# Optimization experiments

Hardware: AMD Instinct MI355X
Metric: run time of the kernel (lower is better)

## Reference

```python
import jax, jax.numpy as jnp
import numpy as np

B, C, N = 4, 256, 4096
OUT = 256
TEMP = OUT ** 0.5  # temperature = sqrt(out_channel)


def setup_inputs() -> dict:
    key = jax.random.key(0)
    kx, kxx, kq, kk, kv = jax.random.split(key, 5)
    x = jax.random.normal(kx, (B, C, N), dtype=jnp.float32)
    xx = jax.random.normal(kxx, (B, C, N), dtype=jnp.float32)
    # Conv1d(in, out, kernel=1, bias=False) weights, squeezed to (out, in)
    s = 1.0 / np.sqrt(C)
    Wq = jax.random.uniform(kq, (OUT, C), jnp.float32, -s, s)
    Wk = jax.random.uniform(kk, (OUT, C), jnp.float32, -s, s)
    Wv = jax.random.uniform(kv, (OUT, C), jnp.float32, -s, s)
    return {"x": x, "xx": xx, "Wq": Wq, "Wk": Wk, "Wv": Wv}


def reference(x, xx, Wq, Wk, Wv):
    # 1x1 conv == per-point linear: (out,in) x (b,in,n) -> (b,out,n)
    q = jnp.einsum('oc,bcn->bon', Wq, x)
    k = jnp.einsum('oc,bcn->bon', Wk, xx)
    v = jnp.einsum('oc,bcn->bon', Wv, xx)
    # attn = (q^T / temp) @ k : (B, N, N)
    attn = jax.nn.softmax(jnp.einsum('bon,bom->bnm', q, k) / TEMP, axis=-1)
    # dropout is identity in eval mode
    # y = attn @ v^T -> (B, N, OUT); returned transposed to (B, OUT, N)
    y = jnp.einsum('bnm,bom->bon', attn, v)
    return y
```

## Files before the change

kernel.cpp:

```cpp
#include <hip/hip_runtime.h>
#include <hip/hip_bf16.h>


typedef __attribute__((ext_vector_type(8))) short bf16x8;
typedef __attribute__((ext_vector_type(4))) float f32x4;
typedef __attribute__((ext_vector_type(4))) short short4t;

constexpr int B_ = 4;
constexpr int C_ = 256;
constexpr int N_ = 4096;
constexpr int O_ = 256;
constexpr float INV_TEMP = 1.0f / 16.0f;
constexpr int NIT = 64;

__device__ __forceinline__ short f2bf(float f) {
  union { float f; unsigned u; } v; v.f = f;
  unsigned r = v.u + 0x7fffu + ((v.u >> 16) & 1u);
  return (short)(r >> 16);
}

__device__ __forceinline__ void dma16(const short* g, short* l) {
  __builtin_amdgcn_global_load_lds(
      (const __attribute__((address_space(1))) unsigned int*)g,
      (__attribute__((address_space(3))) unsigned int*)l, 16, 0, 0);
}

__global__ void wcvt(const float* __restrict__ Wq, const float* __restrict__ Wk,
                     const float* __restrict__ Wv, short* __restrict__ wb) {
  int i = blockIdx.x * 256 + threadIdx.x;
  int mat = i >> 16, off = i & 65535;
  const float* W = (mat == 0) ? Wq : (mat == 1 ? Wk : Wv);
  wb[i] = f2bf(W[off]);
}

__global__ __launch_bounds__(256, 2) void qkv_proj(
    const float* __restrict__ x, const float* __restrict__ xx,
    const short* __restrict__ wb,
    short* __restrict__ qg, short* __restrict__ kt, short* __restrict__ vt) {
  const int n0  = blockIdx.x * 64;
  const int b   = blockIdx.y;
  const int mat = blockIdx.z;
  const float* src = (mat == 0) ? x : xx;
  const short* W   = wb + mat * 65536;
  const int tid = threadIdx.x;
  const int w = tid >> 6, lane = tid & 63;
  const int g = lane >> 4, c16 = lane & 15;

  __shared__ __align__(16) short xs[64][264];

  {
    const int n = tid & 63, cq = tid >> 6;
    const float* sp = src + (size_t)b * C_ * N_ + n0 + n;
#pragma unroll
    for (int rep = 0; rep < 16; ++rep) {
      int c = rep * 16 + cq * 4;
      short4t s4;
#pragma unroll
      for (int j = 0; j < 4; ++j) s4[j] = f2bf(sp[(size_t)(c + j) * N_]);
      *(short4t*)&xs[n][c] = s4;
    }
  }
  __syncthreads();

  f32x4 acc[4][4];
#pragma unroll
  for (int i = 0; i < 4; ++i)
#pragma unroll
    for (int j = 0; j < 4; ++j) acc[i][j] = (f32x4){0.f, 0.f, 0.f, 0.f};

#pragma unroll
  for (int ko = 0; ko < 8; ++ko) {
    bf16x8 wfr[4], xfr[4];
#pragma unroll
    for (int ot = 0; ot < 4; ++ot)
      wfr[ot] = *(const bf16x8*)&W[(w * 64 + ot * 16 + c16) * C_ + ko * 32 + g * 8];
#pragma unroll
    for (int nt = 0; nt < 4; ++nt)
      xfr[nt] = *(const bf16x8*)&xs[nt * 16 + c16][ko * 32 + g * 8];
    if (mat < 2) {
#pragma unroll
      for (int ot = 0; ot < 4; ++ot)
#pragma unroll
        for (int nt = 0; nt < 4; ++nt)
          acc[ot][nt] = __builtin_amdgcn_mfma_f32_16x16x32_bf16(
              wfr[ot], xfr[nt], acc[ot][nt], 0, 0, 0);
    } else {
#pragma unroll
      for (int mt = 0; mt < 4; ++mt)
#pragma unroll
        for (int ot = 0; ot < 4; ++ot)
          acc[mt][ot] = __builtin_amdgcn_mfma_f32_16x16x32_bf16(
              xfr[mt], wfr[ot], acc[mt][ot], 0, 0, 0);
    }
  }

  __syncthreads();
  short* ob = &xs[0][0];

  if (mat == 0) {
#pragma unroll
    for (int ot = 0; ot < 4; ++ot)
#pragma unroll
      for (int nt = 0; nt < 4; ++nt) {
        int f = (nt * 16 + c16) * 256 + w * 64 + ot * 16 + g * 4;
        short4t s;
        s[0] = f2bf(acc[ot][nt][0] * INV_TEMP);
        s[1] = f2bf(acc[ot][nt][1] * INV_TEMP);
        s[2] = f2bf(acc[ot][nt][2] * INV_TEMP);
        s[3] = f2bf(acc[ot][nt][3] * INV_TEMP);
        *(short4t*)&ob[f] = s;
      }
  } else if (mat == 1) {
#pragma unroll
    for (int ot = 0; ot < 4; ++ot)
#pragma unroll
      for (int nt = 0; nt < 4; ++nt) {
        int koo = w * 2 + (ot >> 1);
        int pos = (((ot & 1) * 2 + (g >> 1)) ^ ((c16 >> 1) & 3));
        int f = nt * 4096 + koo * 512 + c16 * 32 + pos * 8 + (g & 1) * 4;
        short4t s;
        s[0] = f2bf(acc[ot][nt][0]);
        s[1] = f2bf(acc[ot][nt][1]);
        s[2] = f2bf(acc[ot][nt][2]);
        s[3] = f2bf(acc[ot][nt][3]);
        *(short4t*)&ob[f] = s;
      }
  } else {
#pragma unroll
    for (int mt = 0; mt < 4; ++mt)
#pragma unroll
      for (int ot = 0; ot < 4; ++ot) {
        int o = w * 64 + ot * 16 + c16;
        int pos = (mt * 2 + (g >> 1)) ^ (o & 7);
        int f = o * 64 + pos * 8 + (g & 1) * 4;
        short4t s;
        s[0] = f2bf(acc[mt][ot][0]);
        s[1] = f2bf(acc[mt][ot][1]);
        s[2] = f2bf(acc[mt][ot][2]);
        s[3] = f2bf(acc[mt][ot][3]);
        *(short4t*)&ob[f] = s;
      }
  }
  __syncthreads();

  short* dst = (mat == 0) ? qg + ((size_t)b * N_ + n0) * O_
             : (mat == 1) ? kt + (size_t)(b * 256 + (n0 >> 4)) * 4096
                          : vt + (size_t)(b * 64 + (n0 >> 6)) * 16384;
  const uint4* s4 = (const uint4*)ob;
  uint4* d4 = (uint4*)dst;
#pragma unroll
  for (int j = 0; j < 8; ++j) d4[j * 256 + tid] = s4[j * 256 + tid];
}

__global__ __launch_bounds__(512, 2) void flash_attn(
    const short* __restrict__ qg, const short* __restrict__ kt,
    const short* __restrict__ vt, float* __restrict__ out) {
  const int xg = blockIdx.x;
  const int b  = xg >> 1;
  const int n0 = (((xg & 1) << 5) + blockIdx.y) * 64;
  const int tid = threadIdx.x;
  const int w = tid >> 6, lane = tid & 63;
  const int g = lane >> 4, c16 = lane & 15;
  const bool prod = (w < 4);
  const int pw = w & 3;

  __shared__ short kb[2][16384];
  __shared__ short vb[2][16384];
  __shared__ short ps[2][64][72];
  __shared__ float lsum[4][64];

  const short* ktb = kt + (size_t)b * N_ * O_;
  const short* vtb = vt + (size_t)b * N_ * O_;

  bf16x8 qf[4][8];
  float lrun[4] = {0.f, 0.f, 0.f, 0.f};
  f32x4 oacc[4][4];
#pragma unroll
  for (int i = 0; i < 4; ++i)
#pragma unroll
    for (int j = 0; j < 4; ++j) oacc[i][j] = (f32x4){0.f, 0.f, 0.f, 0.f};

  if (prod) {
#pragma unroll
    for (int nt = 0; nt < 4; ++nt) {
      const short* qrow =
          qg + (size_t)(b * N_ + n0 + nt * 16 + c16) * O_ + g * 8;
#pragma unroll
      for (int ko = 0; ko < 8; ++ko)
        qf[nt][ko] = *(const bf16x8*)(qrow + ko * 32);
    }
    const short* src = ktb + (size_t)pw * 4096;
#pragma unroll
    for (int j = 0; j < 8; ++j)
      dma16(src + j * 512 + lane * 8, &kb[0][pw * 4096 + j * 512]);
  }
  __syncthreads();

  const int sw = (g ^ ((c16 >> 1) & 3)) * 8;

  for (int i = 0; i <= NIT; ++i) {
    if (prod) {
      if (i < NIT) {
        if (i + 1 < NIT) {
          const short* src = ktb + (size_t)(4 * (i + 1) + pw) * 4096;
          short* dst = &kb[(i + 1) & 1][pw * 4096];
#pragma unroll
          for (int j = 0; j < 8; ++j)
            dma16(src + j * 512 + lane * 8, dst + j * 512);
        }
        const short* ksl = &kb[i & 1][pw * 4096];
        f32x4 sacc[4];
#pragma unroll
        for (int nt = 0; nt < 4; ++nt) sacc[nt] = (f32x4){0.f, 0.f, 0.f, 0.f};
#pragma unroll
        for (int ko = 0; ko < 8; ++ko) {
          bf16x8 kf = *(const bf16x8*)&ksl[(ko * 16 + c16) * 32 + sw];
#pragma unroll
          for (int nt = 0; nt < 4; ++nt)
            sacc[nt] = __builtin_amdgcn_mfma_f32_16x16x32_bf16(
                kf, qf[nt][ko], sacc[nt], 0, 0, 0);
        }
#pragma unroll
        for (int nt = 0; nt < 4; ++nt) {
          short4t pb;
          float rs = 0.f;
#pragma unroll
          for (int r = 0; r < 4; ++r) {
            float p = __expf(sacc[nt][r]);
            rs += p;
            pb[r] = f2bf(p);
          }
          lrun[nt] += rs;
          *(short4t*)&ps[i & 1][nt * 16 + c16][pw * 16 + g * 4] = pb;
        }
      }
    } else {
      if (i < NIT) {
        const short* src = vtb + (size_t)i * 16384 + pw * 4096;
        short* dst = &vb[i & 1][pw * 4096];
#pragma unroll
        for (int j = 0; j < 8; ++j)
          dma16(src + j * 512 + lane * 8, dst + j * 512);
      }
      if (i > 0) {
        const int pb_ = (i - 1) & 1;
#pragma unroll
        for (int kk = 0; kk < 2; ++kk) {
          bf16x8 pf[4];
#pragma unroll
          for (int nt = 0; nt < 4; ++nt)
            pf[nt] = *(const bf16x8*)&ps[pb_][nt * 16 + c16][kk * 32 + g * 8];
#pragma unroll
          for (int ot = 0; ot < 4; ++ot) {
            int pos = (kk * 4 + g) ^ (c16 & 7);
            bf16x8 vf = *(const bf16x8*)
                &vb[pb_][(pw * 64 + ot * 16 + c16) * 64 + pos * 8];
#pragma unroll
            for (int nt = 0; nt < 4; ++nt)
              oacc[ot][nt] = __builtin_amdgcn_mfma_f32_16x16x32_bf16(
                  vf, pf[nt], oacc[ot][nt], 0, 0, 0);
          }
        }
      }
    }
    __syncthreads();
  }

  if (prod) {
#pragma unroll
    for (int nt = 0; nt < 4; ++nt) {
      float v = lrun[nt];
      v += __shfl_xor(v, 16);
      v += __shfl_xor(v, 32);
      if (lane < 16) lsum[pw][nt * 16 + lane] = v;
    }
  }
  __syncthreads();
  if (!prod) {
#pragma unroll
    for (int nt = 0; nt < 4; ++nt) {
      const int nl = nt * 16 + c16;
      float l = lsum[0][nl] + lsum[1][nl] + lsum[2][nl] + lsum[3][nl];
      float li = 1.0f / l;
#pragma unroll
      for (int ot = 0; ot < 4; ++ot) {
        float* op = out + ((size_t)b * O_ + pw * 64 + ot * 16 + g * 4) * N_ +
                    n0 + nl;
#pragma unroll
        for (int r = 0; r < 4; ++r)
          op[(size_t)r * N_] = oacc[ot][nt][r] * li;
      }
    }
  }
}

extern "C" void kernel_launch(void* const* d_in, const int* in_sizes, int n_in,
                              void* d_out, int out_size, void* d_ws,
                              size_t ws_size, hipStream_t stream) {
  const float* x  = (const float*)d_in[0];
  const float* xx = (const float*)d_in[1];
  const float* Wq = (const float*)d_in[2];
  const float* Wk = (const float*)d_in[3];
  const float* Wv = (const float*)d_in[4];
  float* out = (float*)d_out;

  short* qg = (short*)d_ws;
  short* kt = qg + (size_t)B_ * N_ * O_;
  short* vt = kt + (size_t)B_ * N_ * O_;
  short* wb = vt + (size_t)B_ * N_ * O_;

  wcvt<<<768, 256, 0, stream>>>(Wq, Wk, Wv, wb);
  qkv_proj<<<dim3(N_ / 64, B_, 3), 256, 0, stream>>>(x, xx, wb, qg, kt, vt);
  flash_attn<<<dim3(8, 32), 512, 0, stream>>>(qg, kt, vt, out);
}
```

Before: 207.3 us.

## Fuse weight conversion, QKV projection and flash attention into one cooperative kernel

Result: slower. 254.7 us (+22.9%).

```diff
diff --git a/kernel.cpp b/kernel.cpp
--- a/kernel.cpp
+++ b/kernel.cpp
@@ -1,6 +1,9 @@
 #include <hip/hip_runtime.h>
 #include <hip/hip_bf16.h>
-
+#include <hip/hip_cooperative_groups.h>
+
+
+namespace cg = cooperative_groups;
 
 typedef __attribute__((ext_vector_type(8))) short bf16x8;
 typedef __attribute__((ext_vector_type(4))) float f32x4;
@@ -19,155 +22,178 @@
   return (short)(r >> 16);
 }
 
-__device__ __forceinline__ void dma16(const short* g, short* l) {
+__device__ __forceinline__ void dma16(const void* g, void* l) {
   __builtin_amdgcn_global_load_lds(
       (const __attribute__((address_space(1))) unsigned int*)g,
       (__attribute__((address_space(3))) unsigned int*)l, 16, 0, 0);
 }
 
-__global__ void wcvt(const float* __restrict__ Wq, const float* __restrict__ Wk,
-                     const float* __restrict__ Wv, short* __restrict__ wb) {
-  int i = blockIdx.x * 256 + threadIdx.x;
-  int mat = i >> 16, off = i & 65535;
-  const float* W = (mat == 0) ? Wq : (mat == 1 ? Wk : Wv);
-  wb[i] = f2bf(W[off]);
-}
-
-__global__ __launch_bounds__(256, 2) void qkv_proj(
-    const float* __restrict__ x, const float* __restrict__ xx,
-    const short* __restrict__ wb,
-    short* __restrict__ qg, short* __restrict__ kt, short* __restrict__ vt) {
-  const int n0  = blockIdx.x * 64;
-  const int b   = blockIdx.y;
-  const int mat = blockIdx.z;
-  const float* src = (mat == 0) ? x : xx;
-  const short* W   = wb + mat * 65536;
-  const int tid = threadIdx.x;
-  const int w = tid >> 6, lane = tid & 63;
-  const int g = lane >> 4, c16 = lane & 15;
-
-  __shared__ __align__(16) short xs[64][264];
-
-  {
-    const int n = tid & 63, cq = tid >> 6;
-    const float* sp = src + (size_t)b * C_ * N_ + n0 + n;
-#pragma unroll
-    for (int rep = 0; rep < 16; ++rep) {
-      int c = rep * 16 + cq * 4;
-      short4t s4;
-#pragma unroll
-      for (int j = 0; j < 4; ++j) s4[j] = f2bf(sp[(size_t)(c + j) * N_]);
-      *(short4t*)&xs[n][c] = s4;
-    }
-  }
-  __syncthreads();
-
-  f32x4 acc[4][4];
-#pragma unroll
-  for (int i = 0; i < 4; ++i)
-#pragma unroll
-    for (int j = 0; j < 4; ++j) acc[i][j] = (f32x4){0.f, 0.f, 0.f, 0.f};
-
+__device__ __forceinline__ void proj_gemm(
+    const float* __restrict__ Wm, float ws, int swap, const short (*xs)[264],
+    int W4, int oh, int g, int c16, f32x4* a) {
+#pragma unroll
+  for (int i = 0; i < 8; ++i) a[i] = (f32x4){0.f, 0.f, 0.f, 0.f};
 #pragma unroll
   for (int ko = 0; ko < 8; ++ko) {
-    bf16x8 wfr[4], xfr[4];
-#pragma unroll
-    for (int ot = 0; ot < 4; ++ot)
-      wfr[ot] = *(const bf16x8*)&W[(w * 64 + ot * 16 + c16) * C_ + ko * 32 + g * 8];
+    bf16x8 wfr[2], xfr[4];
+#pragma unroll
+    for (int otl = 0; otl < 2; ++otl) {
+      const float* wp = Wm +
+          (size_t)(W4 * 64 + (oh * 2 + otl) * 16 + c16) * C_ + ko * 32 + g * 8;
+      float4 f0 = *(const float4*)wp;
+      float4 f1 = *(const float4*)(wp + 4);
+      bf16x8 t;
+      t[0] = f2bf(f0.x * ws); t[1] = f2bf(f0.y * ws);
+      t[2] = f2bf(f0.z * ws); t[3] = f2bf(f0.w * ws);
+      t[4] = f2bf(f1.x * ws); t[5] = f2bf(f1.y * ws);
+      t[6] = f2bf(f1.z * ws); t[7] = f2bf(f1.w * ws);
+      wfr[otl] = t;
+    }
 #pragma unroll
     for (int nt = 0; nt < 4; ++nt)
       xfr[nt] = *(const bf16x8*)&xs[nt * 16 + c16][ko * 32 + g * 8];
-    if (mat < 2) {
-#pragma unroll
-      for (int ot = 0; ot < 4; ++ot)
+    if (!swap) {
+#pragma unroll
+      for (int otl = 0; otl < 2; ++otl)
 #pragma unroll
         for (int nt = 0; nt < 4; ++nt)
-          acc[ot][nt] = __builtin_amdgcn_mfma_f32_16x16x32_bf16(
-              wfr[ot], xfr[nt], acc[ot][nt], 0, 0, 0);
+          a[otl * 4 + nt] = __builtin_amdgcn_mfma_f32_16x16x32_bf16(
+              wfr[otl], xfr[nt], a[otl * 4 + nt], 0, 0, 0);
     } else {
 #pragma unroll
       for (int mt = 0; mt < 4; ++mt)
 #pragma unroll
-        for (int ot = 0; ot < 4; ++ot)
-          acc[mt][ot] = __builtin_amdgcn_mfma_f32_16x16x32_bf16(
-              xfr[mt], wfr[ot], acc[mt][ot], 0, 0, 0);
-    }
-  }
-
-  __syncthreads();
-  short* ob = &xs[0][0];
-
-  if (mat == 0) {
-#pragma unroll
-    for (int ot = 0; ot < 4; ++ot)
-#pragma unroll
-      for (int nt = 0; nt < 4; ++nt) {
-        int f = (nt * 16 + c16) * 256 + w * 64 + ot * 16 + g * 4;
-        short4t s;
-        s[0] = f2bf(acc[ot][nt][0] * INV_TEMP);
-        s[1] = f2bf(acc[ot][nt][1] * INV_TEMP);
-        s[2] = f2bf(acc[ot][nt][2] * INV_TEMP);
-        s[3] = f2bf(acc[ot][nt][3] * INV_TEMP);
-        *(short4t*)&ob[f] = s;
-      }
-  } else if (mat == 1) {
-#pragma unroll
-    for (int ot = 0; ot < 4; ++ot)
-#pragma unroll
-      for (int nt = 0; nt < 4; ++nt) {
-        int koo = w * 2 + (ot >> 1);
-        int pos = (((ot & 1) * 2 + (g >> 1)) ^ ((c16 >> 1) & 3));
-        int f = nt * 4096 + koo * 512 + c16 * 32 + pos * 8 + (g & 1) * 4;
-        short4t s;
-        s[0] = f2bf(acc[ot][nt][0]);
-        s[1] = f2bf(acc[ot][nt][1]);
-        s[2] = f2bf(acc[ot][nt][2]);
-        s[3] = f2bf(acc[ot][nt][3]);
-        *(short4t*)&ob[f] = s;
-      }
-  } else {
-#pragma unroll
-    for (int mt = 0; mt < 4; ++mt)
-#pragma unroll
-      for (int ot = 0; ot < 4; ++ot) {
-        int o = w * 64 + ot * 16 + c16;
-        int pos = (mt * 2 + (g >> 1)) ^ (o & 7);
-        int f = o * 64 + pos * 8 + (g & 1) * 4;
-        short4t s;
-        s[0] = f2bf(acc[mt][ot][0]);
-        s[1] = f2bf(acc[mt][ot][1]);
-        s[2] = f2bf(acc[mt][ot][2]);
-        s[3] = f2bf(acc[mt][ot][3]);
-        *(short4t*)&ob[f] = s;
-      }
-  }
-  __syncthreads();
-
-  short* dst = (mat == 0) ? qg + ((size_t)b * N_ + n0) * O_
-             : (mat == 1) ? kt + (size_t)(b * 256 + (n0 >> 4)) * 4096
-                          : vt + (size_t)(b * 64 + (n0 >> 6)) * 16384;
-  const uint4* s4 = (const uint4*)ob;
-  uint4* d4 = (uint4*)dst;
-#pragma unroll
-  for (int j = 0; j < 8; ++j) d4[j * 256 + tid] = s4[j * 256 + tid];
-}
-
-__global__ __launch_bounds__(512, 2) void flash_attn(
-    const short* __restrict__ qg, const short* __restrict__ kt,
-    const short* __restrict__ vt, float* __restrict__ out) {
+        for (int otl = 0; otl < 2; ++otl)
+          a[mt * 2 + otl] = __builtin_amdgcn_mfma_f32_16x16x32_bf16(
+              xfr[mt], wfr[otl], a[mt * 2 + otl], 0, 0, 0);
+    }
+  }
+}
+
+__global__ __launch_bounds__(512, 2) void fused(
+    const float* __restrict__ x, const float* __restrict__ xx,
+    const float* __restrict__ Wq, const float* __restrict__ Wk,
+    const float* __restrict__ Wv,
+    short* __restrict__ qg, short* __restrict__ kt, short* __restrict__ vt,
+    float* __restrict__ out) {
   const int xg = blockIdx.x;
   const int b  = xg >> 1;
   const int n0 = (((xg & 1) << 5) + blockIdx.y) * 64;
   const int tid = threadIdx.x;
   const int w = tid >> 6, lane = tid & 63;
   const int g = lane >> 4, c16 = lane & 15;
-  const bool prod = (w < 4);
-  const int pw = w & 3;
 
   __shared__ short kb[2][16384];
   __shared__ short vb[2][16384];
   __shared__ short ps[2][64][72];
   __shared__ float lsum[4][64];
+
+  {
+    short (*xs)[264] = (short(*)[264])&kb[0][0];
+    short* obuf = &vb[0][0];
+    const int W4 = w & 3, oh = w >> 2;
+    f32x4 a[8];
+
+    {
+      const int n = tid & 63, cq = tid >> 6;
+      const float* sp = x + (size_t)b * C_ * N_ + n0 + n;
+#pragma unroll
+      for (int rep = 0; rep < 8; ++rep) {
+        int c = rep * 32 + cq * 4;
+        short4t s4;
+#pragma unroll
+        for (int j = 0; j < 4; ++j) s4[j] = f2bf(sp[(size_t)(c + j) * N_]);
+        *(short4t*)&xs[n][c] = s4;
+      }
+    }
+    __syncthreads();
+
+    proj_gemm(Wq, INV_TEMP, 0, xs, W4, oh, g, c16, a);
+    __syncthreads();
+    {
+#pragma unroll
+      for (int otl = 0; otl < 2; ++otl)
+#pragma unroll
+        for (int nt = 0; nt < 4; ++nt) {
+          int f = (nt * 16 + c16) * 256 + W4 * 64 + (oh * 2 + otl) * 16 + g * 4;
+          f32x4 v = a[otl * 4 + nt];
+          short4t s;
+          s[0] = f2bf(v[0]); s[1] = f2bf(v[1]);
+          s[2] = f2bf(v[2]); s[3] = f2bf(v[3]);
+          *(short4t*)&obuf[f] = s;
+        }
+      const int n = tid & 63, cq = tid >> 6;
+      const float* sp = xx + (size_t)b * C_ * N_ + n0 + n;
+#pragma unroll
+      for (int rep = 0; rep < 8; ++rep) {
+        int c = rep * 32 + cq * 4;
+        short4t s4;
+#pragma unroll
+        for (int j = 0; j < 4; ++j) s4[j] = f2bf(sp[(size_t)(c + j) * N_]);
+        *(short4t*)&xs[n][c] = s4;
+      }
+    }
+    __syncthreads();
+    {
+      const uint4* s4 = (const uint4*)obuf;
+      uint4* d4 = (uint4*)(qg + ((size_t)b * N_ + n0) * O_);
+#pragma unroll
+      for (int j = 0; j < 4; ++j) d4[j * 512 + tid] = s4[j * 512 + tid];
+      proj_gemm(Wk, 1.0f, 0, xs, W4, oh, g, c16, a);
+    }
+    __syncthreads();
+    {
+#pragma unroll
+      for (int otl = 0; otl < 2; ++otl)
+#pragma unroll
+        for (int nt = 0; nt < 4; ++nt) {
+          int koo = W4 * 2 + oh;
+          int pos = ((otl * 2 + (g >> 1)) ^ ((c16 >> 1) & 3));
+          int f = nt * 4096 + koo * 512 + c16 * 32 + pos * 8 + (g & 1) * 4;
+          f32x4 v = a[otl * 4 + nt];
+          short4t s;
+          s[0] = f2bf(v[0]); s[1] = f2bf(v[1]);
+          s[2] = f2bf(v[2]); s[3] = f2bf(v[3]);
+          *(short4t*)&obuf[f] = s;
+        }
+    }
+    __syncthreads();
+    {
+      const uint4* s4 = (const uint4*)obuf;
+      uint4* d4 = (uint4*)(kt + (size_t)(b * 256 + (n0 >> 4)) * 4096);
+#pragma unroll
+      for (int j = 0; j < 4; ++j) d4[j * 512 + tid] = s4[j * 512 + tid];
+      proj_gemm(Wv, 1.0f, 1, xs, W4, oh, g, c16, a);
+    }
+    __syncthreads();
+    {
+#pragma unroll
+      for (int mt = 0; mt < 4; ++mt)
+#pragma unroll
+        for (int otl = 0; otl < 2; ++otl) {
+          int o = W4 * 64 + (oh * 2 + otl) * 16 + c16;
+          int pos = (mt * 2 + (g >> 1)) ^ (o & 7);
+          int f = o * 64 + pos * 8 + (g & 1) * 4;
+          f32x4 v = a[mt * 2 + otl];
+          short4t s;
+          s[0] = f2bf(v[0]); s[1] = f2bf(v[1]);
+          s[2] = f2bf(v[2]); s[3] = f2bf(v[3]);
+          *(short4t*)&obuf[f] = s;
+        }
+    }
+    __syncthreads();
+    {
+      const uint4* s4 = (const uint4*)obuf;
+      uint4* d4 = (uint4*)(vt + (size_t)(b * 64 + (n0 >> 6)) * 16384);
+#pragma unroll
+      for (int j = 0; j < 4; ++j) d4[j * 512 + tid] = s4[j * 512 + tid];
+    }
+  }
+
+  cg::this_grid().sync();
+
+  const bool prod = (w < 4);
+  const int pw = w & 3;
 
   const short* ktb = kt + (size_t)b * N_ * O_;
   const short* vtb = vt + (size_t)b * N_ * O_;
@@ -307,9 +333,9 @@
   short* qg = (short*)d_ws;
   short* kt = qg + (size_t)B_ * N_ * O_;
   short* vt = kt + (size_t)B_ * N_ * O_;
-  short* wb = vt + (size_t)B_ * N_ * O_;
-
-  wcvt<<<768, 256, 0, stream>>>(Wq, Wk, Wv, wb);
-  qkv_proj<<<dim3(N_ / 64, B_, 3), 256, 0, stream>>>(x, xx, wb, qg, kt, vt);
-  flash_attn<<<dim3(8, 32), 512, 0, stream>>>(qg, kt, vt, out);
-}
+
+  void* args[] = {(void*)&x, (void*)&xx, (void*)&Wq, (void*)&Wk, (void*)&Wv,
+                  (void*)&qg, (void*)&kt, (void*)&vt, (void*)&out};
+  hipLaunchCooperativeKernel((const void*)fused, dim3(8, 32), dim3(512, 1, 1),
+                             args, 0, stream);
+}
```
